# Kernel tuning notes

Measured on AMD Instinct MI355X. Metric: run time of the kernel, lower is better.

The kernel has to match this reference:

```python
import jax, jax.numpy as jnp
import numpy as np
import math

B, S, E, H, NL, OUT, VOCAB = 16, 512, 1024, 16, 6, 10, 16
D = E // H
PAD = VOCAB - 1
EPS = 1e-5


def _positional_encoding():
    # Faithful to the module: pe[:x.size(0)] indexes the BATCH dim of a
    # [B, S, E] tensor, yielding [B, 1, E] broadcast over sequence.
    pos = jnp.arange(B, dtype=jnp.float32)[:, None]            # [B,1]
    div = jnp.exp(jnp.arange(0, E, 2, dtype=jnp.float32) * (-math.log(10000.0) / E))
    pe = jnp.zeros((B, E), dtype=jnp.float32)
    pe = pe.at[:, 0::2].set(jnp.sin(pos * div))
    pe = pe.at[:, 1::2].set(jnp.cos(pos * div))
    return pe[:, None, :]                                      # [B,1,E]


def setup_inputs() -> dict:
    key = jax.random.key(0)
    ks = jax.random.split(key, 8)
    sc = 0.02
    return {
        "inputs": jax.random.randint(ks[0], (B, S), 0, PAD),   # no pad tokens
        "emb": jax.random.normal(ks[1], (VOCAB, E), jnp.float32) * sc,
        "wq": jax.random.normal(ks[2], (E, E), jnp.float32) * sc,
        "bq": jnp.zeros((E,), jnp.float32),
        "wk": jax.random.normal(ks[3], (E, E), jnp.float32) * sc,
        "bk": jnp.zeros((E,), jnp.float32),
        "wv": jax.random.normal(ks[4], (E, E), jnp.float32) * sc,
        "bv": jnp.zeros((E,), jnp.float32),
        "wfc": jax.random.normal(ks[5], (E, E), jnp.float32) * sc,
        "bfc": jnp.zeros((E,), jnp.float32),
        "gamma": jnp.ones((E,), jnp.float32),
        "beta": jnp.zeros((E,), jnp.float32),
        "wout": jax.random.normal(ks[6], (S * E, OUT), jnp.float32) * sc,
        "bout": jnp.zeros((OUT,), jnp.float32),
    }


def _layernorm(x, gamma, beta):
    mu = jnp.mean(x, axis=-1, keepdims=True)
    var = jnp.mean(jnp.square(x - mu), axis=-1, keepdims=True)
    return (x - mu) * jax.lax.rsqrt(var + EPS) * gamma + beta


def reference(inputs, emb, wq, bq, wk, bk, wv, bv, wfc, bfc, gamma, beta, wout, bout):
    x = emb[inputs]                                            # [B,S,E]
    x = x + (x + _positional_encoding())                       # x += pos_enc(x)
    mask = (inputs == PAD)                                     # [B,S] key-pad mask
    scale = 1.0 / math.sqrt(D)
    for _ in range(NL):  # same (shared) weights each iteration, as in source
        q = (x @ wq + bq).reshape(B, S, H, D).transpose(0, 2, 1, 3)
        k = (x @ wk + bk).reshape(B, S, H, D).transpose(0, 2, 1, 3)
        v = (x @ wv + bv).reshape(B, S, H, D).transpose(0, 2, 1, 3)
        att = jnp.einsum('bhqd,bhkd->bhqk', q, k) * scale      # [B,H,S,S]
        att = jnp.where(mask[:, None, None, :], -jnp.inf, att)
        att = jax.nn.softmax(att, axis=-1)
        o = jnp.einsum('bhqk,bhkd->bhqd', att, v)
        o = o.transpose(0, 2, 1, 3).reshape(B, S, E)
        x = _layernorm(o + x, gamma, beta)                     # dropout = eval identity
        x = _layernorm((x @ wfc + bfc) + x, gamma, beta)
    return x.reshape(B, -1) @ wout + bout                      # [B,OUT]
```

## Files before the change

kernel.cpp:

```cpp
#include <hip/hip_runtime.h>
#include <hip/hip_bf16.h>
#include <math.h>

#define B_   16
#define S_   512
#define E_   1024
#define H_   16
#define D_   64
#define NL_  6
#define OUT_ 10
#define M_   (B_*S_)

typedef short short8 __attribute__((ext_vector_type(8)));
typedef float f32x4 __attribute__((ext_vector_type(4)));
typedef int   int4v __attribute__((ext_vector_type(4)));
typedef unsigned short ushort4v __attribute__((ext_vector_type(4)));

typedef const __attribute__((address_space(1))) unsigned int* gas1_t;
typedef __attribute__((address_space(3))) unsigned int* las3_t;
#define GLD16(g,l) __builtin_amdgcn_global_load_lds((gas1_t)(g), (las3_t)(l), 16, 0, 0)
#define VMW(n) asm volatile("s_waitcnt vmcnt(" #n ")" ::: "memory")

static __device__ __forceinline__ float bf2f(unsigned short u){
  union { unsigned int i; float f; } v; v.i = ((unsigned int)u) << 16; return v.f;
}
static __device__ __forceinline__ unsigned short f2bf(float f){
  union { float f; unsigned int i; } v; v.f = f;
  unsigned int r = v.i + 0x7fffu + ((v.i >> 16) & 1u);
  return (unsigned short)(r >> 16);
}
static __device__ __forceinline__ f32x4 mfma16(short8 a, short8 b, f32x4 c){
  return __builtin_amdgcn_mfma_f32_16x16x32_bf16(a, b, c, 0, 0, 0);
}

__global__ __launch_bounds__(192)
void code_k(float* __restrict__ out, float code)
{
  int t = threadIdx.x;
  if (t < B_*OUT_) out[t] = code;
}

__global__ __launch_bounds__(256)
void transpose_k(const float* __restrict__ w0, const float* __restrict__ w1,
                 const float* __restrict__ w2, const float* __restrict__ w3,
                 unsigned short* __restrict__ wT)
{
  const float* w = blockIdx.z==0 ? w0 : blockIdx.z==1 ? w1 : blockIdx.z==2 ? w2 : w3;
  unsigned short* o = wT + (size_t)blockIdx.z * E_ * E_;
  __shared__ unsigned short tl[64][65];
  int n0 = blockIdx.x*64, k0 = blockIdx.y*64;
  int tx = threadIdx.x, ty = threadIdx.y;
  #pragma unroll
  for (int i = 0; i < 16; ++i)
    tl[ty + 4*i][tx] = f2bf(w[(size_t)(k0 + ty + 4*i)*E_ + n0 + tx]);
  __syncthreads();
  #pragma unroll
  for (int i = 0; i < 16; ++i)
    o[(size_t)(n0 + ty + 4*i)*E_ + k0 + tx] = tl[tx][ty + 4*i];
}

__global__ __launch_bounds__(256)
void embed_k(const int* __restrict__ tok, const float* __restrict__ emb,
             float* __restrict__ x, unsigned short* __restrict__ xb)
{
  int row = blockIdx.x;
  int b = row >> 9;
  int tk = tok[row];
  tk = tk < 0 ? 0 : (tk > 15 ? 15 : tk);
  int e0 = threadIdx.x * 4;
  const float c0 = -9.210340371976184f / (float)E_;
  f32x4 ev = *(const f32x4*)&emb[(size_t)tk * E_ + e0];
  f32x4 vv; ushort4v bb;
  #pragma unroll
  for (int i = 0; i < 4; ++i) {
    int e = e0 + i;
    float dv = expf((float)(e & ~1) * c0);
    float arg = (float)b * dv;
    float pe = (e & 1) ? cosf(arg) : sinf(arg);
    float v = 2.0f * ev[i] + pe;
    vv[i] = v; bb[i] = f2bf(v);
  }
  *(f32x4*)&x[(size_t)row*E_ + e0] = vv;
  *(ushort4v*)&xb[(size_t)row*E_ + e0] = bb;
}

template<int MODE>
__global__ __launch_bounds__(512, 2)
void gemm256_k(const unsigned short* __restrict__ A,
               const unsigned short* __restrict__ WT,
               const float* __restrict__ bq, const float* __restrict__ bk,
               const float* __restrict__ bv,
               unsigned short* __restrict__ out)
{
  extern __shared__ unsigned short SM2[];
  int mt = blockIdx.x, nt = blockIdx.y;
  int wsel = (MODE==0) ? (nt>>2) : 3;
  int ntl  = (MODE==0) ? (nt&3)  : nt;
  const unsigned short* Bp = WT + (MODE==0 ? (size_t)wsel*E_*E_ : (size_t)0) + (size_t)ntl*256*E_;
  const float* bias = (MODE==0) ? (wsel==0 ? bq : (wsel==1 ? bk : bv)) : bq;
  int m0 = mt*128;
  int tid = threadIdx.x, lane = tid&63, wid = tid>>6;
  int lr = lane&15, lk = lane>>4;
  int rl = tid>>3;
  int cs = (tid&7) ^ (rl&7);

  unsigned short *a0 = SM2,          *a1 = SM2 + 8192,  *a2 = SM2 + 16384;
  unsigned short *b0 = SM2 + 24576,  *b1 = SM2 + 40960, *b2 = SM2 + 57344;

  f32x4 acc[8][2] = {};

  auto stA = [&](unsigned short* dst, int kt) {
    GLD16(A + (size_t)(m0 + rl)*E_ + kt*64 + cs*8,      dst + (tid<<3));
    GLD16(A + (size_t)(m0 + 64 + rl)*E_ + kt*64 + cs*8, dst + ((512 + tid)<<3));
  };
  auto stB = [&](unsigned short* dst, int kt) {
    GLD16(Bp + (size_t)(rl)*E_ + kt*64 + cs*8,       dst + (tid<<3));
    GLD16(Bp + (size_t)(64 + rl)*E_ + kt*64 + cs*8,  dst + ((512 + tid)<<3));
    GLD16(Bp + (size_t)(128 + rl)*E_ + kt*64 + cs*8, dst + ((1024 + tid)<<3));
    GLD16(Bp + (size_t)(192 + rl)*E_ + kt*64 + cs*8, dst + ((1536 + tid)<<3));
  };

  stB(b0, 0); stA(a0, 0);
  stB(b1, 1); stA(a1, 1);

  int sw0 = (lk ^ (lr&7)) * 8;
  int sw1 = ((4+lk) ^ (lr&7)) * 8;
  for (int kt = 0; kt < 16; ++kt) {
    #pragma unroll
    for (int p = 0; p < 2; ++p) {
      if (p == 0) {
        if (kt < 14)      { stB(b2, kt+2); VMW(11); }
        else if (kt == 14) VMW(7);
        else               VMW(1);
      } else {
        if (kt < 14)      { stA(a2, kt+2); VMW(12); }
        else if (kt == 14) VMW(6);
        else               VMW(0);
      }
      __builtin_amdgcn_s_barrier();
      short8 af[4][2], bfr[2][2];
      #pragma unroll
      for (int i = 0; i < 4; ++i) {
        int row = (p*4 + i)*16 + lr;
        af[i][0] = *(const short8*)&a0[row*64 + sw0];
        af[i][1] = *(const short8*)&a0[row*64 + sw1];
      }
      #pragma unroll
      for (int ni = 0; ni < 2; ++ni) {
        int row = wid*32 + ni*16 + lr;
        bfr[ni][0] = *(const short8*)&b0[row*64 + sw0];
        bfr[ni][1] = *(const short8*)&b0[row*64 + sw1];
      }
      __builtin_amdgcn_s_setprio(1);
      #pragma unroll
      for (int kk = 0; kk < 2; ++kk)
        #pragma unroll
        for (int i = 0; i < 4; ++i)
          #pragma unroll
          for (int ni = 0; ni < 2; ++ni)
            acc[p*4+i][ni] = mfma16(af[i][kk], bfr[ni][kk], acc[p*4+i][ni]);
      __builtin_amdgcn_s_setprio(0);
      __builtin_amdgcn_s_barrier();
    }
    unsigned short* ta = a0; a0 = a1; a1 = a2; a2 = ta;
    unsigned short* tb = b0; b0 = b1; b1 = b2; b2 = tb;
  }

  if (MODE == 1 || wsel < 2) {
    unsigned short* Cs = SM2;
    #pragma unroll
    for (int ni = 0; ni < 2; ++ni) {
      int n = ntl*256 + wid*32 + ni*16 + lr;
      float bv2 = bias[n];
      #pragma unroll
      for (int mi = 0; mi < 8; ++mi)
        #pragma unroll
        for (int j = 0; j < 4; ++j)
          Cs[(mi*16 + lk*4 + j)*272 + wid*32 + ni*16 + lr] =
            f2bf(acc[mi][ni][j] + bv2);
    }
    __syncthreads();
    int r = tid >> 2, qd = tid & 3;
    const unsigned short* sp = &Cs[r*272 + qd*64];
    unsigned short* gp;
    if (MODE == 1) {
      gp = out + (size_t)(m0 + r)*E_ + ntl*256 + qd*64;
    } else {
      int m = m0 + r;
      int b = m >> 9, s = m & 511;
      int h = ntl*4 + qd;
      gp = out + (size_t)wsel*M_*E_ + (((size_t)(b*H_ + h)*S_ + s)*D_);
    }
    #pragma unroll
    for (int c = 0; c < 8; ++c)
      *(int4v*)(gp + c*8) = *(const int4v*)(sp + c*8);
  } else {
    unsigned short* Ct = SM2;
    #pragma unroll
    for (int ni = 0; ni < 2; ++ni) {
      int nl = wid*32 + ni*16 + lr;
      float bv2 = bias[ntl*256 + nl];
      #pragma unroll
      for (int mi = 0; mi < 8; ++mi)
        #pragma unroll
        for (int j = 0; j < 4; ++j)
          Ct[nl*136 + mi*16 + lk*4 + j] = f2bf(acc[mi][ni][j] + bv2);
    }
    __syncthreads();
    int nl = tid >> 1, half = tid & 1;
    int n = ntl*256 + nl;
    int h = n >> 6, d = n & 63;
    int b = m0 >> 9, s0 = m0 & 511;
    unsigned short* gp = out + (size_t)2*M_*E_ +
                         (((size_t)(b*H_ + h)*D_ + d)*S_ + s0 + half*64);
    const unsigned short* sp = &Ct[nl*136 + half*64];
    #pragma unroll
    for (int c = 0; c < 8; ++c)
      *(int4v*)(gp + c*8) = *(const int4v*)(sp + c*8);
  }
}

__global__ __launch_bounds__(512, 4)
void attn_k(const unsigned short* __restrict__ Q, const unsigned short* __restrict__ K,
            const unsigned short* __restrict__ VT, unsigned short* __restrict__ O)
{
  extern __shared__ unsigned short SMEM[];
  int bid = blockIdx.x;
  int bh = bid & 255, qh = bid >> 8;
  int tid = threadIdx.x, lane = tid & 63, wid = tid >> 6;
  int lr = lane & 15, lk = lane >> 4;
  const unsigned short* Qb = Q + (size_t)bh * S_ * D_;
  const unsigned short* Kb = K + (size_t)bh * S_ * D_;
  const unsigned short* VTb = VT + (size_t)bh * S_ * D_;
  unsigned short* Pw = SMEM + 32768 + wid * 640;

  int kr  = tid >> 3, kc8 = tid & 7;
  int kcs = kc8 ^ (kr & 7);
  short8 qf[2][2];
  #pragma unroll
  for (int s = 0; s < 2; ++s) {
    int q0 = (qh*2 + s)*128 + wid*16;
    qf[s][0] = *(const short8*)(Qb + (size_t)(q0 + lr)*D_ + lk*8);
    qf[s][1] = *(const short8*)(Qb + (size_t)(q0 + lr)*D_ + 32 + lk*8);
  }
  {
    unsigned short* Kd = SMEM;
    #pragma unroll
    for (int j = 0; j < 2; ++j) {
      int idx = j*512 + tid;
      GLD16(Kb + (size_t)(kr + j*64)*D_ + kcs*8, &Kd[idx*8]);
    }
  }
  {
    unsigned short* Vd = SMEM + 16384;
    #pragma unroll
    for (int j = 0; j < 2; ++j) {
      int idx = j*512 + tid;
      int d = idx >> 4, c16 = idx & 15;
      int cds = c16 ^ (d & 15);
      GLD16(VTb + (size_t)d*S_ + cds*8, &Vd[idx*8]);
    }
  }
  __syncthreads();

  f32x4 oacc[2][4] = {};
  float plsum[2][4] = {{0.f,0.f,0.f,0.f},{0.f,0.f,0.f,0.f}};
  int cur = 0;
  for (int kt = 0; kt < 4; ++kt) {
    if (kt < 3) {
      unsigned short* Kd = SMEM + (cur^1)*8192;
      unsigned short* Vd = SMEM + 16384 + (cur^1)*8192;
      #pragma unroll
      for (int j = 0; j < 2; ++j) {
        int idx = j*512 + tid;
        int r = idx >> 3, c8 = idx & 7;
        GLD16(Kb + (size_t)((kt+1)*128 + r)*D_ + (c8 ^ (r & 7))*8, &Kd[idx*8]);
        int d = idx >> 4, c16 = idx & 15;
        GLD16(VTb + (size_t)d*S_ + (kt+1)*128 + (c16 ^ (d & 15))*8, &Vd[idx*8]);
      }
    }
    const unsigned short* Kl = SMEM + cur*8192;
    const unsigned short* Vl = SMEM + 16384 + cur*8192;
    #pragma unroll
    for (int s = 0; s < 2; ++s) {
      #pragma unroll
      for (int c = 0; c < 4; ++c) {
        f32x4 s0 = {}, s1 = {};
        {
          const unsigned short* kr0 = &Kl[((2*c)*16 + lr)*64];
          const unsigned short* kr1 = &Kl[((2*c+1)*16 + lr)*64];
          int a0 = ((lk     ^ (lr & 7)))*8;
          int a1 = (((4+lk) ^ (lr & 7)))*8;
          s0 = mfma16(qf[s][0], *(const short8*)(kr0 + a0), s0);
          s0 = mfma16(qf[s][1], *(const short8*)(kr0 + a1), s0);
          s1 = mfma16(qf[s][0], *(const short8*)(kr1 + a0), s1);
          s1 = mfma16(qf[s][1], *(const short8*)(kr1 + a1), s1);
        }
        #pragma unroll
        for (int j = 0; j < 4; ++j) {
          s0[j] = __expf(s0[j] * 0.125f);
          s1[j] = __expf(s1[j] * 0.125f);
          plsum[s][j] += s0[j] + s1[j];
        }
        #pragma unroll
        for (int j = 0; j < 4; ++j) {
          Pw[(lk*4 + j)*40 + lr]      = f2bf(s0[j]);
          Pw[(lk*4 + j)*40 + 16 + lr] = f2bf(s1[j]);
        }
        asm volatile("s_waitcnt lgkmcnt(0)" ::: "memory");
        short8 pf = *(const short8*)&Pw[lr*40 + lk*8];
        #pragma unroll
        for (int dt = 0; dt < 4; ++dt) {
          int drow = dt*16 + lr;
          short8 vf = *(const short8*)&Vl[drow*128 + (((c*4 + lk) ^ lr))*8];
          oacc[s][dt] = mfma16(pf, vf, oacc[s][dt]);
        }
      }
    }
    __syncthreads();
    cur ^= 1;
  }
  #pragma unroll
  for (int s = 0; s < 2; ++s) {
    float lsum[4];
    #pragma unroll
    for (int j = 0; j < 4; ++j) {
      float t = plsum[s][j];
      #pragma unroll
      for (int m = 1; m < 16; m <<= 1) t += __shfl_xor(t, m);
      lsum[j] = t;
    }
    int q0 = (qh*2 + s)*128 + wid*16;
    #pragma unroll
    for (int dt = 0; dt < 4; ++dt)
      #pragma unroll
      for (int j = 0; j < 4; ++j)
        O[(size_t)bh*S_*D_ + (size_t)(q0 + lk*4 + j)*D_ + dt*16 + lr] =
          f2bf(oacc[s][dt][j] / lsum[j]);
  }
}

template<bool PERM>
__global__ __launch_bounds__(256)
void ln_k(const unsigned short* __restrict__ g, float* __restrict__ x,
          unsigned short* __restrict__ xb,
          const float* __restrict__ gamma, const float* __restrict__ beta)
{
  int row = blockIdx.x;
  int tid = threadIdx.x;
  int e0 = tid * 4;
  ushort4v gu;
  if (PERM) {
    int b = row >> 9, s = row & 511;
    int h = e0 >> 6, d = e0 & 63;
    gu = *(const ushort4v*)&g[(((size_t)(b*H_ + h)*S_) + s)*D_ + d];
  } else {
    gu = *(const ushort4v*)&g[(size_t)row*E_ + e0];
  }
  f32x4 xv = *(const f32x4*)&x[(size_t)row*E_ + e0];
  f32x4 v;
  #pragma unroll
  for (int i = 0; i < 4; ++i) v[i] = bf2f(gu[i]) + xv[i];
  float sum = v[0]+v[1]+v[2]+v[3];
  float sq  = v[0]*v[0]+v[1]*v[1]+v[2]*v[2]+v[3]*v[3];
  #pragma unroll
  for (int m = 1; m < 64; m <<= 1) { sum += __shfl_xor(sum, m); sq += __shfl_xor(sq, m); }
  __shared__ float red[2][4];
  int lane = tid & 63, wid = tid >> 6;
  if (lane == 0) { red[0][wid] = sum; red[1][wid] = sq; }
  __syncthreads();
  float ts = red[0][0]+red[0][1]+red[0][2]+red[0][3];
  float tq = red[1][0]+red[1][1]+red[1][2]+red[1][3];
  float mu = ts * (1.0f/E_);
  float var = tq * (1.0f/E_) - mu*mu;
  float rsq = rsqrtf(var + 1e-5f);
  f32x4 y; ushort4v yb;
  #pragma unroll
  for (int i = 0; i < 4; ++i) {
    float t = (v[i]-mu)*rsq*gamma[e0+i] + beta[e0+i];
    y[i] = t; yb[i] = f2bf(t);
  }
  *(f32x4*)&x[(size_t)row*E_ + e0] = y;
  *(ushort4v*)&xb[(size_t)row*E_ + e0] = yb;
}

__global__ __launch_bounds__(256)
void outp_k(const float* __restrict__ x, const float* __restrict__ wout,
            float* __restrict__ part)
{
  int b = blockIdx.y;
  int chunk = blockIdx.x;
  int tid = threadIdx.x;
  float acc[OUT_] = {};
  const float* xr = x + (size_t)b * S_ * E_;
  for (int j = 0; j < 32; ++j) {
    int k = chunk*8192 + j*256 + tid;
    float xv = xr[k];
    const float* wr = wout + (size_t)k * OUT_;
    #pragma unroll
    for (int o = 0; o < OUT_; ++o) acc[o] += xv * wr[o];
  }
  #pragma unroll
  for (int o = 0; o < OUT_; ++o)
    #pragma unroll
    for (int m = 1; m < 64; m <<= 1) acc[o] += __shfl_xor(acc[o], m);
  __shared__ float red[4][OUT_];
  int lane = tid & 63, wid = tid >> 6;
  if (lane == 0) {
    #pragma unroll
    for (int o = 0; o < OUT_; ++o) red[wid][o] = acc[o];
  }
  __syncthreads();
  if (tid < OUT_) {
    float s = red[0][tid] + red[1][tid] + red[2][tid] + red[3][tid];
    part[((size_t)chunk*B_ + b)*OUT_ + tid] = s;
  }
}

__global__ __launch_bounds__(192)
void outred_k(const float* __restrict__ part, const float* __restrict__ bout,
              float* __restrict__ out)
{
  int t = threadIdx.x;
  if (t < B_*OUT_) {
    int b = t / OUT_, o = t % OUT_;
    float s = 0.f;
    for (int c = 0; c < 64; ++c) s += part[((size_t)c*B_ + b)*OUT_ + o];
    s += bout[o];
    out[t] = s;
  }
}

extern "C" void kernel_launch(void* const* d_in, const int* in_sizes, int n_in,
                              void* d_out, int out_size, void* d_ws, size_t ws_size,
                              hipStream_t stream)
{
  (void)out_size;
  float* outb = (float*)d_out;

  static const int expect[14] = {8192, 16384, 1048576, 1024, 1048576, 1024,
                                 1048576, 1024, 1048576, 1024, 1024, 1024,
                                 5242880, 10};
  if (n_in != 14) { code_k<<<dim3(1), dim3(192), 0, stream>>>(outb, 9000.0f); return; }
  for (int i = 0; i < 14; ++i)
    if (in_sizes[i] != expect[i]) {
      code_k<<<dim3(1), dim3(192), 0, stream>>>(outb, 5000.0f + 100.0f*i); return;
    }

  const int* tok = (const int*)d_in[0];
  const float* emb  = (const float*)d_in[1];
  const float* wq   = (const float*)d_in[2];
  const float* bq   = (const float*)d_in[3];
  const float* wk   = (const float*)d_in[4];
  const float* bk   = (const float*)d_in[5];
  const float* wv   = (const float*)d_in[6];
  const float* bv   = (const float*)d_in[7];
  const float* wfc  = (const float*)d_in[8];
  const float* bfc  = (const float*)d_in[9];
  const float* gam  = (const float*)d_in[10];
  const float* bet  = (const float*)d_in[11];
  const float* wout = (const float*)d_in[12];
  const float* bout = (const float*)d_in[13];

  char* ws = (char*)d_ws;
  size_t off = 0;
  unsigned short* wT = (unsigned short*)(ws + off); off += (size_t)4*E_*E_*2;
  float* x  = (float*)(ws + off);                   off += (size_t)M_*E_*4;
  unsigned short* xb = (unsigned short*)(ws + off); off += (size_t)M_*E_*2;
  unsigned short* qkvb = (unsigned short*)(ws + off); off += (size_t)3*M_*E_*2;
  unsigned short* gb = (unsigned short*)(ws + off); off += (size_t)M_*E_*2;
  float* part = (float*)(ws + off);                 off += (size_t)64*B_*OUT_*4;
  if (off > ws_size) { code_k<<<dim3(1), dim3(192), 0, stream>>>(outb, 9500.0f); return; }

  transpose_k<<<dim3(16,16,4), dim3(64,4), 0, stream>>>(wq, wk, wv, wfc, wT);
  embed_k<<<dim3(M_), dim3(256), 0, stream>>>(tok, emb, x, xb);
  unsigned short* qb = qkvb;
  unsigned short* kb = qkvb + (size_t)M_*E_;
  unsigned short* vb = qkvb + (size_t)2*M_*E_;
  for (int l = 0; l < NL_; ++l) {
    gemm256_k<0><<<dim3(64,12), dim3(512), 147456, stream>>>(xb, wT, bq, bk, bv, qkvb);
    attn_k<<<dim3(512), dim3(512), 75776, stream>>>(qb, kb, vb, gb);
    ln_k<true><<<dim3(M_), dim3(256), 0, stream>>>(gb, x, xb, gam, bet);
    gemm256_k<1><<<dim3(64,4), dim3(512), 147456, stream>>>(xb, wT + (size_t)3*E_*E_, bfc, bfc, bfc, gb);
    ln_k<false><<<dim3(M_), dim3(256), 0, stream>>>(gb, x, xb, gam, bet);
  }
  outp_k<<<dim3(64,B_), dim3(256), 0, stream>>>(x, wout, part);
  outred_k<<<dim3(1), dim3(192), 0, stream>>>(part, bout, outb);
}
```

Measured before the change: 1.038 ms.

## Enlarge GEMM tile to 256x256 with 2x4 warp grid and double buffering

The projection GEMM block tile grows from 128x256 to 256x256. Each of the 8 waves now owns a 128x64 sub-tile in a 2x4 grid instead of a 128x32 column strip, which raises arithmetic intensity per LDS load and halves the grid size. The triple-buffered LDS pipeline becomes double-buffered, with the next B tile's loads spread across the inner phases. The trade-off is more accumulator registers (32 f32x4 per thread), which may hurt occupancy. With 128 and 384 blocks there may also be too few blocks to fill the device's compute units.

```diff
diff --git a/kernel.cpp b/kernel.cpp
--- a/kernel.cpp
+++ b/kernel.cpp
@@ -98,125 +98,143 @@
   int ntl  = (MODE==0) ? (nt&3)  : nt;
   const unsigned short* Bp = WT + (MODE==0 ? (size_t)wsel*E_*E_ : (size_t)0) + (size_t)ntl*256*E_;
   const float* bias = (MODE==0) ? (wsel==0 ? bq : (wsel==1 ? bk : bv)) : bq;
-  int m0 = mt*128;
+  int m0 = mt*256;
   int tid = threadIdx.x, lane = tid&63, wid = tid>>6;
+  int wr = wid>>2, wc = wid&3;
   int lr = lane&15, lk = lane>>4;
   int rl = tid>>3;
   int cs = (tid&7) ^ (rl&7);
-
-  unsigned short *a0 = SM2,          *a1 = SM2 + 8192,  *a2 = SM2 + 16384;
-  unsigned short *b0 = SM2 + 24576,  *b1 = SM2 + 40960, *b2 = SM2 + 57344;
-
-  f32x4 acc[8][2] = {};
+  int sw0 = (lk ^ (lr&7)) << 3;
+  int sw1 = ((4+lk) ^ (lr&7)) << 3;
+
+  unsigned short* Ab0 = SM2;
+  unsigned short* Ab1 = SM2 + 16384;
+  unsigned short* Bb0 = SM2 + 32768;
+  unsigned short* Bb1 = SM2 + 49152;
+
+  f32x4 acc[8][4] = {};
 
   auto stA = [&](unsigned short* dst, int kt) {
-    GLD16(A + (size_t)(m0 + rl)*E_ + kt*64 + cs*8,      dst + (tid<<3));
-    GLD16(A + (size_t)(m0 + 64 + rl)*E_ + kt*64 + cs*8, dst + ((512 + tid)<<3));
+    #pragma unroll
+    for (int q = 0; q < 4; ++q)
+      GLD16(A + (size_t)(m0 + q*64 + rl)*E_ + kt*64 + cs*8, dst + ((q*512 + tid)<<3));
   };
-  auto stB = [&](unsigned short* dst, int kt) {
-    GLD16(Bp + (size_t)(rl)*E_ + kt*64 + cs*8,       dst + (tid<<3));
-    GLD16(Bp + (size_t)(64 + rl)*E_ + kt*64 + cs*8,  dst + ((512 + tid)<<3));
-    GLD16(Bp + (size_t)(128 + rl)*E_ + kt*64 + cs*8, dst + ((1024 + tid)<<3));
-    GLD16(Bp + (size_t)(192 + rl)*E_ + kt*64 + cs*8, dst + ((1536 + tid)<<3));
+  auto stBh = [&](unsigned short* dst, int kt, int h) {
+    GLD16(Bp + (size_t)(h*128 + rl)*E_ + kt*64 + cs*8,      dst + ((h*1024 + tid)<<3));
+    GLD16(Bp + (size_t)(h*128 + 64 + rl)*E_ + kt*64 + cs*8, dst + ((h*1024 + 512 + tid)<<3));
   };
 
-  stB(b0, 0); stA(a0, 0);
-  stB(b1, 1); stA(a1, 1);
-
-  int sw0 = (lk ^ (lr&7)) * 8;
-  int sw1 = ((4+lk) ^ (lr&7)) * 8;
+  stA(Ab0, 0); stBh(Bb0, 0, 0); stBh(Bb0, 0, 1);
+
   for (int kt = 0; kt < 16; ++kt) {
-    #pragma unroll
-    for (int p = 0; p < 2; ++p) {
+    int cur = kt & 1;
+    const unsigned short* Ar = cur ? Ab1 : Ab0;
+    const unsigned short* Br = cur ? Bb1 : Bb0;
+    unsigned short* An = cur ? Ab0 : Ab1;
+    unsigned short* Bn = cur ? Bb0 : Bb1;
+    short8 bfr[4][2];
+    #pragma unroll
+    for (int p = 0; p < 4; ++p) {
+      short8 af[2][2];
       if (p == 0) {
-        if (kt < 14)      { stB(b2, kt+2); VMW(11); }
-        else if (kt == 14) VMW(7);
-        else               VMW(1);
+        if (kt < 15) { stA(An, kt+1); VMW(4); }
+        else         { VMW(0); }
+        __builtin_amdgcn_s_barrier();
+        #pragma unroll
+        for (int i = 0; i < 2; ++i) {
+          int row = wr*128 + i*16 + lr;
+          af[i][0] = *(const short8*)&Ar[row*64 + sw0];
+          af[i][1] = *(const short8*)&Ar[row*64 + sw1];
+        }
+        #pragma unroll
+        for (int ni = 0; ni < 4; ++ni) {
+          int row = wc*64 + ni*16 + lr;
+          bfr[ni][0] = *(const short8*)&Br[row*64 + sw0];
+          bfr[ni][1] = *(const short8*)&Br[row*64 + sw1];
+        }
       } else {
-        if (kt < 14)      { stA(a2, kt+2); VMW(12); }
-        else if (kt == 14) VMW(6);
-        else               VMW(0);
-      }
-      __builtin_amdgcn_s_barrier();
-      short8 af[4][2], bfr[2][2];
-      #pragma unroll
-      for (int i = 0; i < 4; ++i) {
-        int row = (p*4 + i)*16 + lr;
-        af[i][0] = *(const short8*)&a0[row*64 + sw0];
-        af[i][1] = *(const short8*)&a0[row*64 + sw1];
-      }
-      #pragma unroll
-      for (int ni = 0; ni < 2; ++ni) {
-        int row = wid*32 + ni*16 + lr;
-        bfr[ni][0] = *(const short8*)&b0[row*64 + sw0];
-        bfr[ni][1] = *(const short8*)&b0[row*64 + sw1];
+        #pragma unroll
+        for (int i = 0; i < 2; ++i) {
+          int row = wr*128 + (p*2 + i)*16 + lr;
+          af[i][0] = *(const short8*)&Ar[row*64 + sw0];
+          af[i][1] = *(const short8*)&Ar[row*64 + sw1];
+        }
+        if (p == 1 && kt < 15) stBh(Bn, kt+1, 0);
+        if (p == 2 && kt < 15) stBh(Bn, kt+1, 1);
+        __builtin_amdgcn_s_barrier();
       }
       __builtin_amdgcn_s_setprio(1);
       #pragma unroll
       for (int kk = 0; kk < 2; ++kk)
         #pragma unroll
-        for (int i = 0; i < 4; ++i)
+        for (int i = 0; i < 2; ++i)
           #pragma unroll
-          for (int ni = 0; ni < 2; ++ni)
-            acc[p*4+i][ni] = mfma16(af[i][kk], bfr[ni][kk], acc[p*4+i][ni]);
+          for (int ni = 0; ni < 4; ++ni)
+            acc[p*2+i][ni] = mfma16(af[i][kk], bfr[ni][kk], acc[p*2+i][ni]);
       __builtin_amdgcn_s_setprio(0);
       __builtin_amdgcn_s_barrier();
     }
-    unsigned short* ta = a0; a0 = a1; a1 = a2; a2 = ta;
-    unsigned short* tb = b0; b0 = b1; b1 = b2; b2 = tb;
   }
 
   if (MODE == 1 || wsel < 2) {
     unsigned short* Cs = SM2;
     #pragma unroll
-    for (int ni = 0; ni < 2; ++ni) {
-      int n = ntl*256 + wid*32 + ni*16 + lr;
+    for (int ni = 0; ni < 4; ++ni) {
+      int n = ntl*256 + wc*64 + ni*16 + lr;
       float bv2 = bias[n];
       #pragma unroll
       for (int mi = 0; mi < 8; ++mi)
         #pragma unroll
         for (int j = 0; j < 4; ++j)
-          Cs[(mi*16 + lk*4 + j)*272 + wid*32 + ni*16 + lr] =
+          Cs[(wr*128 + mi*16 + lk*4 + j)*272 + wc*64 + ni*16 + lr] =
             f2bf(acc[mi][ni][j] + bv2);
     }
     __syncthreads();
-    int r = tid >> 2, qd = tid & 3;
-    const unsigned short* sp = &Cs[r*272 + qd*64];
-    unsigned short* gp;
-    if (MODE == 1) {
-      gp = out + (size_t)(m0 + r)*E_ + ntl*256 + qd*64;
-    } else {
-      int m = m0 + r;
-      int b = m >> 9, s = m & 511;
-      int h = ntl*4 + qd;
-      gp = out + (size_t)wsel*M_*E_ + (((size_t)(b*H_ + h)*S_ + s)*D_);
-    }
-    #pragma unroll
-    for (int c = 0; c < 8; ++c)
-      *(int4v*)(gp + c*8) = *(const int4v*)(sp + c*8);
+    #pragma unroll
+    for (int it = 0; it < 2; ++it) {
+      int id = it*512 + tid;
+      int r = id >> 2, qd = id & 3;
+      const unsigned short* sp = &Cs[r*272 + qd*64];
+      unsigned short* gp;
+      if (MODE == 1) {
+        gp = out + (size_t)(m0 + r)*E_ + ntl*256 + qd*64;
+      } else {
+        int m = m0 + r;
+        int b = m >> 9, s = m & 511;
+        int h = ntl*4 + qd;
+        gp = out + (size_t)wsel*M_*E_ + (((size_t)(b*H_ + h)*S_ + s)*D_);
+      }
+      #pragma unroll
+      for (int c = 0; c < 8; ++c)
+        *(int4v*)(gp + c*8) = *(const int4v*)(sp + c*8);
+    }
   } else {
     unsigned short* Ct = SM2;
     #pragma unroll
-    for (int ni = 0; ni < 2; ++ni) {
-      int nl = wid*32 + ni*16 + lr;
+    for (int ni = 0; ni < 4; ++ni) {
+      int nl = wc*64 + ni*16 + lr;
       float bv2 = bias[ntl*256 + nl];
       #pragma unroll
       for (int mi = 0; mi < 8; ++mi)
         #pragma unroll
         for (int j = 0; j < 4; ++j)
-          Ct[nl*136 + mi*16 + lk*4 + j] = f2bf(acc[mi][ni][j] + bv2);
+          Ct[nl*264 + wr*128 + mi*16 + lk*4 + j] = f2bf(acc[mi][ni][j] + bv2);
     }
     __syncthreads();
-    int nl = tid >> 1, half = tid & 1;
-    int n = ntl*256 + nl;
-    int h = n >> 6, d = n & 63;
     int b = m0 >> 9, s0 = m0 & 511;
-    unsigned short* gp = out + (size_t)2*M_*E_ +
-                         (((size_t)(b*H_ + h)*D_ + d)*S_ + s0 + half*64);
-    const unsigned short* sp = &Ct[nl*136 + half*64];
-    #pragma unroll
-    for (int c = 0; c < 8; ++c)
-      *(int4v*)(gp + c*8) = *(const int4v*)(sp + c*8);
+    #pragma unroll
+    for (int it = 0; it < 2; ++it) {
+      int id = it*512 + tid;
+      int nl = id >> 2, mc = id & 3;
+      int n = ntl*256 + nl;
+      int h = n >> 6, d = n & 63;
+      unsigned short* gp = out + (size_t)2*M_*E_ +
+                           (((size_t)(b*H_ + h)*D_ + d)*S_ + s0 + mc*64);
+      const unsigned short* sp = &Ct[nl*264 + mc*64];
+      #pragma unroll
+      for (int c = 0; c < 8; ++c)
+        *(int4v*)(gp + c*8) = *(const int4v*)(sp + c*8);
+    }
   }
 }
 
@@ -478,10 +496,10 @@
   unsigned short* kb = qkvb + (size_t)M_*E_;
   unsigned short* vb = qkvb + (size_t)2*M_*E_;
   for (int l = 0; l < NL_; ++l) {
-    gemm256_k<0><<<dim3(64,12), dim3(512), 147456, stream>>>(xb, wT, bq, bk, bv, qkvb);
+    gemm256_k<0><<<dim3(32,12), dim3(512), 147456, stream>>>(xb, wT, bq, bk, bv, qkvb);
     attn_k<<<dim3(512), dim3(512), 75776, stream>>>(qb, kb, vb, gb);
     ln_k<true><<<dim3(M_), dim3(256), 0, stream>>>(gb, x, xb, gam, bet);
-    gemm256_k<1><<<dim3(64,4), dim3(512), 147456, stream>>>(xb, wT + (size_t)3*E_*E_, bfc, bfc, bfc, gb);
+    gemm256_k<1><<<dim3(32,4), dim3(512), 147456, stream>>>(xb, wT + (size_t)3*E_*E_, bfc, bfc, bfc, gb);
     ln_k<false><<<dim3(M_), dim3(256), 0, stream>>>(gb, x, xb, gam, bet);
   }
   outp_k<<<dim3(64,B_), dim3(256), 0, stream>>>(x, wout, part);
```

New measurement: 1.082 ms. 4.2% more time.
